# Kernel tuning notes

Hardware: AMD Instinct MI355X
Metric: run time of the kernel (lower is better)

## Reference

```python
import jax, jax.numpy as jnp
import numpy as np

D_MODEL = 768
NHEAD = 12
D_K = D_MODEL // NHEAD
D_FF = 3072
EPS = 1e-6


def layer_norm(x, a, b):
    # torch LayerNorm here: mean/std over last dim, std is UNBIASED (n-1), eps added to std
    n = x.shape[-1]
    m = jnp.mean(x, axis=-1, keepdims=True)
    var = jnp.sum((x - m) ** 2, axis=-1, keepdims=True) / (n - 1)
    return a * (x - m) / (jnp.sqrt(var) + EPS) + b


def setup_inputs() -> dict:
    key = jax.random.key(0)
    ks = jax.random.split(key, 12)
    B, S = 2, 2048
    s = 1.0 / np.sqrt(D_MODEL)
    inp = {
        'x': jax.random.normal(ks[0], (B, S, D_MODEL), jnp.float32),
        'mask': jnp.ones((B, 1, S), jnp.int32),
        'Wq': jax.random.normal(ks[1], (D_MODEL, D_MODEL), jnp.float32) * s,
        'bq': jnp.zeros((D_MODEL,), jnp.float32),
        'Wk': jax.random.normal(ks[2], (D_MODEL, D_MODEL), jnp.float32) * s,
        'bk': jnp.zeros((D_MODEL,), jnp.float32),
        'Wv': jax.random.normal(ks[3], (D_MODEL, D_MODEL), jnp.float32) * s,
        'bv': jnp.zeros((D_MODEL,), jnp.float32),
        'Wo': jax.random.normal(ks[4], (D_MODEL, D_MODEL), jnp.float32) * s,
        'bo': jnp.zeros((D_MODEL,), jnp.float32),
        'ln1_a': jnp.ones((D_MODEL,), jnp.float32),
        'ln1_b': jnp.zeros((D_MODEL,), jnp.float32),
        'W1': jax.random.normal(ks[5], (D_MODEL, D_FF), jnp.float32) * s,
        'b1': jnp.zeros((D_FF,), jnp.float32),
        'W2': jax.random.normal(ks[6], (D_FF, D_MODEL), jnp.float32) * (1.0 / np.sqrt(D_FF)),
        'b2': jnp.zeros((D_MODEL,), jnp.float32),
        'ln2_a': jnp.ones((D_MODEL,), jnp.float32),
        'ln2_b': jnp.zeros((D_MODEL,), jnp.float32),
    }
    return inp


def reference(x, mask, Wq, bq, Wk, bk, Wv, bv, Wo, bo, ln1_a, ln1_b, W1, b1, W2, b2, ln2_a, ln2_b):
    B, S, _ = x.shape
    # --- sublayer 1: pre-norm self-attention + residual (dropout = eval/no-op) ---
    h = layer_norm(x, ln1_a, ln1_b)
    q = (h @ Wq + bq).reshape(B, S, NHEAD, D_K).transpose(0, 2, 1, 3)  # [B,H,S,Dk]
    k = (h @ Wk + bk).reshape(B, S, NHEAD, D_K).transpose(0, 2, 1, 3)
    v = (h @ Wv + bv).reshape(B, S, NHEAD, D_K).transpose(0, 2, 1, 3)
    scores = jnp.einsum('bhqd,bhkd->bhqk', q, k) / np.sqrt(D_K)  # [B,H,S,S]
    scores = jnp.where(mask[:, None] == 0, jnp.float32(-1e9), scores)
    attn = jax.nn.softmax(scores, axis=-1)
    ctx = jnp.einsum('bhqk,bhkd->bhqd', attn, v)  # [B,H,S,Dk]
    ctx = ctx.transpose(0, 2, 1, 3).reshape(B, S, D_MODEL)
    x = x + (ctx @ Wo + bo)
    # --- sublayer 2: pre-norm FFN + residual ---
    h2 = layer_norm(x, ln2_a, ln2_b)
    ff = jax.nn.relu(h2 @ W1 + b1) @ W2 + b2
    return x + ff
```

## Files before the change

kernel.cpp:

```cpp
#include <hip/hip_runtime.h>
#include <hip/hip_bf16.h>
#include <stdint.h>

#define DM 768
#define DFF 3072
#define NH 12
#define DK 64
#define SS 2048
#define NTOK 4096
#define KCH 2

typedef __hip_bfloat16 bf16;
typedef short bf16x8 __attribute__((ext_vector_type(8)));
typedef float f32x4 __attribute__((ext_vector_type(4)));

#define MFMA16(a, b, c) __builtin_amdgcn_mfma_f32_16x16x32_bf16((a), (b), (c), 0, 0, 0)

#define QSCALE 0.18033688011112042f

#if __has_builtin(__builtin_amdgcn_exp2f)
#define EXP2F(x) __builtin_amdgcn_exp2f(x)
#else
#define EXP2F(x) exp2f(x)
#endif

static __device__ __forceinline__ bf16 f2b(float f) { return __float2bfloat16(f); }
static __device__ __forceinline__ unsigned short f2b_bits(float f) {
    bf16 h = __float2bfloat16(f);
    return *reinterpret_cast<unsigned short*>(&h);
}
static __device__ __forceinline__ float b2f(bf16 h) { return __bfloat162float(h); }

static __device__ __forceinline__ void g2l16(const void* g, void* l) {
    __builtin_amdgcn_global_load_lds(
        (const __attribute__((address_space(1))) unsigned int*)g,
        (__attribute__((address_space(3))) unsigned int*)(uintptr_t)l,
        16, 0, 0);
}

__global__ __launch_bounds__(256) void transpose_all(const float* Wq, const float* Wk,
                                                     const float* Wv, const float* Wo,
                                                     const float* W1, const float* W2,
                                                     bf16* WqT, bf16* WkT, bf16* WvT,
                                                     bf16* WoT, bf16* W1T, bf16* W2T) {
    __shared__ float tile[32][33];
    int id = blockIdx.x;
    const float* W; bf16* WT; int K, N, n0, k0;
    if (id < 2304) {
        int z = id / 576, r = id % 576;
        W  = (z == 0) ? Wq : (z == 1) ? Wk : (z == 2) ? Wv : Wo;
        WT = (z == 0) ? WqT : (z == 1) ? WkT : (z == 2) ? WvT : WoT;
        K = 768; N = 768; n0 = (r % 24) * 32; k0 = (r / 24) * 32;
    } else if (id < 4608) {
        int r = id - 2304; W = W1; WT = W1T;
        K = 768; N = 3072; n0 = (r % 96) * 32; k0 = (r / 96) * 32;
    } else {
        int r = id - 4608; W = W2; WT = W2T;
        K = 3072; N = 768; n0 = (r % 24) * 32; k0 = (r / 24) * 32;
    }
    int tx = threadIdx.x & 31, ty = threadIdx.x >> 5;
#pragma unroll
    for (int r = ty; r < 32; r += 8)
        tile[r][tx] = W[(size_t)(k0 + r) * N + n0 + tx];
    __syncthreads();
#pragma unroll
    for (int r = ty; r < 32; r += 8)
        WT[(size_t)(n0 + r) * K + k0 + tx] = f2b(tile[tx][r]);
}

__global__ __launch_bounds__(256) void ln_fwd(const float* __restrict__ x,
                                              const float* __restrict__ g,
                                              const float* __restrict__ be,
                                              bf16* __restrict__ out) {
    int wid = threadIdx.x >> 6, lane = threadIdx.x & 63;
    int row = blockIdx.x * 4 + wid;
    const float* xr = x + (size_t)row * DM;
    float v[12];
    float s = 0.f;
#pragma unroll
    for (int i = 0; i < 12; ++i) { v[i] = xr[lane + i * 64]; s += v[i]; }
#pragma unroll
    for (int off = 32; off >= 1; off >>= 1) s += __shfl_xor(s, off);
    float mean = s * (1.f / 768.f);
    float s2 = 0.f;
#pragma unroll
    for (int i = 0; i < 12; ++i) { float d = v[i] - mean; s2 += d * d; }
#pragma unroll
    for (int off = 32; off >= 1; off >>= 1) s2 += __shfl_xor(s2, off);
    float rstd = 1.f / (sqrtf(s2 * (1.f / 767.f)) + 1e-6f);
    bf16* orow = out + (size_t)row * DM;
#pragma unroll
    for (int i = 0; i < 12; ++i) {
        int c = lane + i * 64;
        orow[c] = f2b(g[c] * (v[i] - mean) * rstd + be[c]);
    }
}

__device__ __forceinline__ void gemm_core(const bf16* __restrict__ A,
                                          const bf16* __restrict__ BT,
                                          int K, int bm, int bn,
                                          bf16* As, bf16* Bs,
                                          f32x4 acc[4][4]) {
    int tid = threadIdx.x;
    int lane = tid & 63, quad = lane >> 4, lid = lane & 15;
    int wid = tid >> 6;
    int wm = (wid >> 1) * 64, wn = (wid & 1) * 64;
    int s0 = tid, s1 = tid + 256;
    int r0 = s0 >> 2, c0 = (s0 & 3) ^ ((r0 >> 1) & 3);
    int r1 = s1 >> 2, c1 = (s1 & 3) ^ ((r1 >> 1) & 3);
    const bf16* A0 = A + (size_t)(bm + r0) * K + c0 * 8;
    const bf16* A1 = A + (size_t)(bm + r1) * K + c1 * 8;
    const bf16* B0 = BT + (size_t)(bn + r0) * K + c0 * 8;
    const bf16* B1 = BT + (size_t)(bn + r1) * K + c1 * 8;
    int rdc = quad ^ ((lid >> 1) & 3);
    g2l16(A0, As + s0 * 8);
    g2l16(B0, Bs + s0 * 8);
    g2l16(A1, As + s1 * 8);
    g2l16(B1, Bs + s1 * 8);
    for (int k0 = 0; k0 < K; k0 += 32) {
        __syncthreads();
        int cur = (k0 >> 5) & 1;
        if (k0 + 32 < K) {
            int nb = (cur ^ 1) * 4096;
            g2l16(A0 + k0 + 32, As + nb + s0 * 8);
            g2l16(B0 + k0 + 32, Bs + nb + s0 * 8);
            g2l16(A1 + k0 + 32, As + nb + s1 * 8);
            g2l16(B1 + k0 + 32, Bs + nb + s1 * 8);
        }
        const bf16* Ac = As + cur * 4096;
        const bf16* Bc = Bs + cur * 4096;
        bf16x8 af[4], bfr[4];
#pragma unroll
        for (int i = 0; i < 4; ++i) af[i]  = *(const bf16x8*)&Ac[(wm + i * 16 + lid) * 32 + rdc * 8];
#pragma unroll
        for (int j = 0; j < 4; ++j) bfr[j] = *(const bf16x8*)&Bc[(wn + j * 16 + lid) * 32 + rdc * 8];
#pragma unroll
        for (int i = 0; i < 4; ++i)
#pragma unroll
            for (int j = 0; j < 4; ++j)
                acc[i][j] = MFMA16(af[i], bfr[j], acc[i][j]);
    }
}

__global__ __launch_bounds__(256) void gemm_qkv(const bf16* __restrict__ A,
                                                const bf16* __restrict__ WqT,
                                                const bf16* __restrict__ WkT,
                                                const bf16* __restrict__ WvT,
                                                const float* __restrict__ bq,
                                                const float* __restrict__ bk,
                                                const float* __restrict__ bv,
                                                bf16* __restrict__ qb,
                                                bf16* __restrict__ kb,
                                                bf16* __restrict__ vtb) {
    __shared__ bf16 As[2 * 128 * 32];
    __shared__ bf16 Bs[2 * 128 * 32];
    int which = blockIdx.x / 6;
    int bn = (blockIdx.x % 6) * 128;
    int bm = blockIdx.y * 128;
    const bf16* BT = (which == 0) ? WqT : (which == 1) ? WkT : WvT;
    const float* bias = (which == 0) ? bq : (which == 1) ? bk : bv;
    f32x4 acc[4][4] = {};
    gemm_core(A, BT, DM, bm, bn, As, Bs, acc);

    int tid = threadIdx.x, wid = tid >> 6, lane = tid & 63, quad = lane >> 4, lid = lane & 15;
    int wm = (wid >> 1) * 64, wn = (wid & 1) * 64;
    float sc = (which == 0) ? QSCALE : 1.f;
#pragma unroll
    for (int j = 0; j < 4; ++j) {
        int col = bn + wn + j * 16 + lid;
        float bb = bias[col];
        int hh = col >> 6, d = col & 63;
#pragma unroll
        for (int i = 0; i < 4; ++i) {
            int rowbase = bm + wm + i * 16 + quad * 4;
            int b = rowbase >> 11;
            int s0 = rowbase & 2047;
            if (which == 2) {
                ushort4 pk;
                pk.x = f2b_bits(acc[i][j][0] + bb);
                pk.y = f2b_bits(acc[i][j][1] + bb);
                pk.z = f2b_bits(acc[i][j][2] + bb);
                pk.w = f2b_bits(acc[i][j][3] + bb);
                *(ushort4*)&vtb[(((size_t)b * NH + hh) * DK + d) * SS + s0] = pk;
            } else {
                bf16* dst = which ? kb : qb;
#pragma unroll
                for (int r = 0; r < 4; ++r)
                    dst[(((size_t)b * NH + hh) * SS + (s0 + r)) * DK + d] = f2b((acc[i][j][r] + bb) * sc);
            }
        }
    }
}

template <int EPI>
__global__ __launch_bounds__(256) void gemm_ep(const bf16* __restrict__ A,
                                               const bf16* __restrict__ BT,
                                               const float* __restrict__ bias,
                                               const float* __restrict__ res,
                                               void* __restrict__ outp,
                                               int N, int K) {
    __shared__ bf16 As[2 * 128 * 32];
    __shared__ bf16 Bs[2 * 128 * 32];
    int bm = blockIdx.y * 128, bn = blockIdx.x * 128;
    f32x4 acc[4][4] = {};
    gemm_core(A, BT, K, bm, bn, As, Bs, acc);

    int tid = threadIdx.x, wid = tid >> 6, lane = tid & 63, quad = lane >> 4, lid = lane & 15;
    int wm = (wid >> 1) * 64, wn = (wid & 1) * 64;
#pragma unroll
    for (int j = 0; j < 4; ++j) {
        int col = bn + wn + j * 16 + lid;
        float bb = bias[col];
#pragma unroll
        for (int i = 0; i < 4; ++i) {
#pragma unroll
            for (int r = 0; r < 4; ++r) {
                int row = bm + wm + i * 16 + quad * 4 + r;
                float v = acc[i][j][r] + bb;
                if (EPI == 2) {
                    ((float*)outp)[(size_t)row * N + col] = res[(size_t)row * N + col] + v;
                } else {
                    ((bf16*)outp)[(size_t)row * N + col] = f2b(fmaxf(v, 0.f));
                }
            }
        }
    }
}

template <int EPI>
__global__ __launch_bounds__(256) void gemm_ep64(const bf16* __restrict__ A,
                                                 const bf16* __restrict__ BT,
                                                 const float* __restrict__ bias,
                                                 const float* __restrict__ res,
                                                 void* __restrict__ outp,
                                                 int N, int K) {
    __shared__ bf16 As[2 * 64 * 32];
    __shared__ bf16 Bs[2 * 128 * 32];
    int bm = blockIdx.y * 64, bn = blockIdx.x * 128;
    int tid = threadIdx.x, wid = tid >> 6, lane = tid & 63, quad = lane >> 4, lid = lane & 15;
    int wm = (wid >> 1) * 32, wn = (wid & 1) * 64;
    f32x4 acc[2][4] = {};
    int ra = tid >> 2, ca = (tid & 3) ^ ((ra >> 1) & 3);
    int s0 = tid, s1 = tid + 256;
    int rb0 = s0 >> 2, cb0 = (s0 & 3) ^ ((rb0 >> 1) & 3);
    int rb1 = s1 >> 2, cb1 = (s1 & 3) ^ ((rb1 >> 1) & 3);
    const bf16* Ap = A + (size_t)(bm + ra) * K + ca * 8;
    const bf16* B0 = BT + (size_t)(bn + rb0) * K + cb0 * 8;
    const bf16* B1 = BT + (size_t)(bn + rb1) * K + cb1 * 8;
    int rdc = quad ^ ((lid >> 1) & 3);
    g2l16(Ap, As + tid * 8);
    g2l16(B0, Bs + s0 * 8);
    g2l16(B1, Bs + s1 * 8);
    for (int k0 = 0; k0 < K; k0 += 32) {
        __syncthreads();
        int cur = (k0 >> 5) & 1;
        if (k0 + 32 < K) {
            g2l16(Ap + k0 + 32, As + (cur ^ 1) * 2048 + tid * 8);
            g2l16(B0 + k0 + 32, Bs + (cur ^ 1) * 4096 + s0 * 8);
            g2l16(B1 + k0 + 32, Bs + (cur ^ 1) * 4096 + s1 * 8);
        }
        const bf16* Ac = As + cur * 2048;
        const bf16* Bc = Bs + cur * 4096;
        bf16x8 af[2], bfr[4];
#pragma unroll
        for (int i = 0; i < 2; ++i) af[i]  = *(const bf16x8*)&Ac[(wm + i * 16 + lid) * 32 + rdc * 8];
#pragma unroll
        for (int j = 0; j < 4; ++j) bfr[j] = *(const bf16x8*)&Bc[(wn + j * 16 + lid) * 32 + rdc * 8];
#pragma unroll
        for (int i = 0; i < 2; ++i)
#pragma unroll
            for (int j = 0; j < 4; ++j)
                acc[i][j] = MFMA16(af[i], bfr[j], acc[i][j]);
    }
#pragma unroll
    for (int j = 0; j < 4; ++j) {
        int col = bn + wn + j * 16 + lid;
        float bb = bias[col];
#pragma unroll
        for (int i = 0; i < 2; ++i) {
#pragma unroll
            for (int r = 0; r < 4; ++r) {
                int row = bm + wm + i * 16 + quad * 4 + r;
                float v = acc[i][j][r] + bb;
                if (EPI == 2) {
                    ((float*)outp)[(size_t)row * N + col] = res[(size_t)row * N + col] + v;
                } else {
                    ((bf16*)outp)[(size_t)row * N + col] = f2b(fmaxf(v, 0.f));
                }
            }
        }
    }
}

__global__ __launch_bounds__(256) void attn_part(const bf16* __restrict__ qb,
                                                 const bf16* __restrict__ kb,
                                                 const bf16* __restrict__ vtb,
                                                 const int* __restrict__ mask,
                                                 bf16* __restrict__ part,
                                                 float* __restrict__ lws) {
    __shared__ bf16 Ks[2 * 64 * 64];
    __shared__ bf16 VTs[2 * 64 * 64];
    __shared__ bf16 Ps[64 * 72];
    int bh = blockIdx.y;
    int b = bh / NH;
    int q0 = blockIdx.x * 64;
    int kc = blockIdx.z;
    const bf16* Kp = kb  + (size_t)bh * SS * DK;
    const bf16* VT = vtb + (size_t)bh * DK * SS;
    int tid = threadIdx.x, wid = tid >> 6, lane = tid & 63, quad = lane >> 4, lid = lane & 15;

    int s0 = tid, s1 = tid + 256;
    int r0 = s0 >> 3, c0 = (s0 & 7) ^ (r0 & 7);
    int r1 = s1 >> 3, c1 = (s1 & 7) ^ (r1 & 7);

    const bf16* Qrow = qb + ((size_t)bh * SS + q0 + wid * 16 + lid) * DK;
    bf16x8 qf0 = *(const bf16x8*)&Qrow[quad * 8];
    bf16x8 qf1 = *(const bf16x8*)&Qrow[32 + quad * 8];

    bf16x8 ones;
#pragma unroll
    for (int i = 0; i < 8; ++i) ones[i] = (short)0x3F80;

    int rdc  = quad ^ (lid & 7);
    int rdc2 = rdc ^ 4;
    const int* mrow = mask + b * SS;

    f32x4 accv[4] = {};
    f32x4 accl = {};

    int tbeg = kc * (SS / 64 / KCH), tend = (kc + 1) * (SS / 64 / KCH);

    {
        int k0 = tbeg * 64;
        g2l16(Kp + (size_t)(k0 + r0) * DK + c0 * 8, Ks + s0 * 8);
        g2l16(Kp + (size_t)(k0 + r1) * DK + c1 * 8, Ks + s1 * 8);
        g2l16(VT + (size_t)r0 * SS + k0 + c0 * 8, VTs + s0 * 8);
        g2l16(VT + (size_t)r1 * SS + k0 + c1 * 8, VTs + s1 * 8);
    }

    int cur = 0;
    for (int t = tbeg; t < tend; ++t) {
        int k0 = t * 64;
        __syncthreads();
        if (t + 1 < tend) {
            int k0n = (t + 1) * 64;
            int nb = (cur ^ 1) * 4096;
            g2l16(Kp + (size_t)(k0n + r0) * DK + c0 * 8, Ks + nb + s0 * 8);
            g2l16(Kp + (size_t)(k0n + r1) * DK + c1 * 8, Ks + nb + s1 * 8);
            g2l16(VT + (size_t)r0 * SS + k0n + c0 * 8, VTs + nb + s0 * 8);
            g2l16(VT + (size_t)r1 * SS + k0n + c1 * 8, VTs + nb + s1 * 8);
        }
        const bf16* Kc  = Ks  + cur * 4096;
        const bf16* VTc = VTs + cur * 4096;

#pragma unroll
        for (int ns = 0; ns < 4; ++ns) {
            bf16x8 kf0 = *(const bf16x8*)&Kc[(ns * 16 + lid) * 64 + rdc * 8];
            bf16x8 kf1 = *(const bf16x8*)&Kc[(ns * 16 + lid) * 64 + rdc2 * 8];
            f32x4 st = {};
            st = MFMA16(kf0, qf0, st);
            st = MFMA16(kf1, qf1, st);
            int4 mk = *(const int4*)&mrow[k0 + ns * 16 + quad * 4];
            float p0 = mk.x ? EXP2F(st[0]) : 0.f;
            float p1 = mk.y ? EXP2F(st[1]) : 0.f;
            float p2 = mk.z ? EXP2F(st[2]) : 0.f;
            float p3 = mk.w ? EXP2F(st[3]) : 0.f;
            __hip_bfloat162 h01 = __float22bfloat162_rn(make_float2(p0, p1));
            __hip_bfloat162 h23 = __float22bfloat162_rn(make_float2(p2, p3));
            uint2 pw;
            pw.x = *(unsigned int*)&h01;
            pw.y = *(unsigned int*)&h23;
            *(uint2*)&Ps[(wid * 16 + lid) * 72 + ns * 16 + quad * 4] = pw;
        }

        bf16x8 pa0 = *(const bf16x8*)&Ps[(wid * 16 + lid) * 72 + quad * 8];
        bf16x8 pa1 = *(const bf16x8*)&Ps[(wid * 16 + lid) * 72 + 32 + quad * 8];

        accl = MFMA16(pa0, ones, accl);
        accl = MFMA16(pa1, ones, accl);

#pragma unroll
        for (int ds = 0; ds < 4; ++ds) {
            bf16x8 vf0 = *(const bf16x8*)&VTc[(ds * 16 + lid) * 64 + rdc * 8];
            bf16x8 vf1 = *(const bf16x8*)&VTc[(ds * 16 + lid) * 64 + rdc2 * 8];
            accv[ds] = MFMA16(pa0, vf0, accv[ds]);
            accv[ds] = MFMA16(pa1, vf1, accv[ds]);
        }
        cur ^= 1;
    }

    if (lid == 0) {
#pragma unroll
        for (int r = 0; r < 4; ++r)
            lws[((size_t)kc * (2 * NH) + bh) * SS + q0 + wid * 16 + quad * 4 + r] = accl[r];
    }

    bf16* pb = part + ((size_t)kc * (2 * NH) + bh) * DK * SS;
    int qbase = q0 + wid * 16 + quad * 4;
#pragma unroll
    for (int ds = 0; ds < 4; ++ds) {
        int d = ds * 16 + lid;
        ushort4 pk;
        pk.x = f2b_bits(accv[ds][0]);
        pk.y = f2b_bits(accv[ds][1]);
        pk.z = f2b_bits(accv[ds][2]);
        pk.w = f2b_bits(accv[ds][3]);
        *(ushort4*)&pb[(size_t)d * SS + qbase] = pk;
    }
}

__global__ __launch_bounds__(256) void attn_combine(const bf16* __restrict__ part,
                                                    const float* __restrict__ lws,
                                                    bf16* __restrict__ ctx) {
    __shared__ float tile[64][66];
    __shared__ float linv[64];
    int bh = blockIdx.y;
    int b = bh / NH, h = bh % NH;
    int q0 = blockIdx.x * 64;
    int tid = threadIdx.x;

    if (tid < 64) {
        float l = 0.f;
#pragma unroll
        for (int kc = 0; kc < KCH; ++kc)
            l += lws[((size_t)kc * (2 * NH) + bh) * SS + q0 + tid];
        linv[tid] = 1.f / l;
    }

    int d = tid >> 2, qs = (tid & 3) * 16;
    const bf16* p0 = part + (((size_t)0 * (2 * NH) + bh) * DK + d) * SS + q0 + qs;
    const bf16* p1 = part + (((size_t)1 * (2 * NH) + bh) * DK + d) * SS + q0 + qs;
    bf16x8 a0 = *(const bf16x8*)p0;
    bf16x8 a1 = *(const bf16x8*)(p0 + 8);
    bf16x8 b0 = *(const bf16x8*)p1;
    bf16x8 b1 = *(const bf16x8*)(p1 + 8);
#pragma unroll
    for (int i = 0; i < 8; ++i) {
        tile[d][qs + i]     = b2f(((const bf16*)&a0)[i]) + b2f(((const bf16*)&b0)[i]);
        tile[d][qs + 8 + i] = b2f(((const bf16*)&a1)[i]) + b2f(((const bf16*)&b1)[i]);
    }
    __syncthreads();

    int q = tid >> 2, ds2 = (tid & 3) * 16;
    float rl = linv[q];
    unsigned int wv[8];
#pragma unroll
    for (int i = 0; i < 8; ++i) {
        __hip_bfloat162 hh = __float22bfloat162_rn(
            make_float2(tile[ds2 + 2 * i][q] * rl, tile[ds2 + 2 * i + 1][q] * rl));
        wv[i] = *(unsigned int*)&hh;
    }
    bf16* crow = ctx + (size_t)(b * SS + q0 + q) * DM + h * DK + ds2;
    uint4 u0 = {wv[0], wv[1], wv[2], wv[3]};
    uint4 u1 = {wv[4], wv[5], wv[6], wv[7]};
    *(uint4*)&crow[0] = u0;
    *(uint4*)&crow[8] = u1;
}

extern "C" void kernel_launch(void* const* d_in, const int* in_sizes, int n_in,
                              void* d_out, int out_size, void* d_ws, size_t ws_size,
                              hipStream_t stream) {
    const float* x    = (const float*)d_in[0];
    const int*   mask = (const int*)d_in[1];
    const float* Wq   = (const float*)d_in[2];
    const float* bq   = (const float*)d_in[3];
    const float* Wk   = (const float*)d_in[4];
    const float* bk   = (const float*)d_in[5];
    const float* Wv   = (const float*)d_in[6];
    const float* bv   = (const float*)d_in[7];
    const float* Wo   = (const float*)d_in[8];
    const float* bo   = (const float*)d_in[9];
    const float* ln1a = (const float*)d_in[10];
    const float* ln1b = (const float*)d_in[11];
    const float* W1   = (const float*)d_in[12];
    const float* b1   = (const float*)d_in[13];
    const float* W2   = (const float*)d_in[14];
    const float* b2   = (const float*)d_in[15];
    const float* ln2a = (const float*)d_in[16];
    const float* ln2b = (const float*)d_in[17];
    float* out = (float*)d_out;

    char* w = (char*)d_ws;
    bf16* h   = (bf16*)w; w += (size_t)NTOK * DM * 2;
    bf16* qb  = (bf16*)w; w += (size_t)NTOK * DM * 2;
    bf16* kb  = (bf16*)w; w += (size_t)NTOK * DM * 2;
    bf16* vtb = (bf16*)w; w += (size_t)NTOK * DM * 2;
    bf16* ctx = (bf16*)w; w += (size_t)NTOK * DM * 2;
    bf16* h2  = (bf16*)w; w += (size_t)NTOK * DM * 2;
    bf16* ffa = (bf16*)w; w += (size_t)NTOK * DFF * 2;
    float* x1 = (float*)w; w += (size_t)NTOK * DM * 4;
    bf16* WqT = (bf16*)w; w += (size_t)DM * DM * 2;
    bf16* WkT = (bf16*)w; w += (size_t)DM * DM * 2;
    bf16* WvT = (bf16*)w; w += (size_t)DM * DM * 2;
    bf16* WoT = (bf16*)w; w += (size_t)DM * DM * 2;
    bf16* W1T = (bf16*)w; w += (size_t)DM * DFF * 2;
    bf16* W2T = (bf16*)w; w += (size_t)DM * DFF * 2;

    bf16*  part = ffa;
    float* lws  = x1;

    transpose_all<<<6912, 256, 0, stream>>>(Wq, Wk, Wv, Wo, W1, W2,
                                            WqT, WkT, WvT, WoT, W1T, W2T);

    ln_fwd<<<NTOK / 4, 256, 0, stream>>>(x, ln1a, ln1b, h);
    gemm_qkv<<<dim3(18, 32), 256, 0, stream>>>(h, WqT, WkT, WvT, bq, bk, bv, qb, kb, vtb);
    attn_part<<<dim3(SS / 64, 2 * NH, KCH), 256, 0, stream>>>(qb, kb, vtb, mask, part, lws);
    attn_combine<<<dim3(SS / 64, 2 * NH), 256, 0, stream>>>(part, lws, ctx);
    gemm_ep64<2><<<dim3(6, 64), 256, 0, stream>>>(ctx, WoT, bo, x, (void*)x1, DM, DM);
    ln_fwd<<<NTOK / 4, 256, 0, stream>>>(x1, ln2a, ln2b, h2);
    gemm_ep<3><<<dim3(24, 32), 256, 0, stream>>>(h2, W1T, b1, nullptr, (void*)ffa, DFF, DM);
    gemm_ep64<2><<<dim3(6, 64), 256, 0, stream>>>(ffa, W2T, b2, x1, (void*)out, DM, DFF);
}
```

Before: 298.8 us.

## Process 128 query rows per attention block to reuse K/V tiles

Each attention_part block now covers 128 queries instead of 64, with every wave computing two 16-row query sub-tiles against each K/V tile staged in shared memory. This halves the global-to-LDS traffic of K and V per query and reuses the K/V fragment reads across two MFMA streams. The grid shrinks to 16x24x2 = 768 blocks, which lowers parallelism on a large-CU GPU, and register pressure rises from the doubled accumulators.

```diff
diff --git a/kernel.cpp b/kernel.cpp
--- a/kernel.cpp
+++ b/kernel.cpp
@@ -300,10 +300,10 @@
                                                  float* __restrict__ lws) {
     __shared__ bf16 Ks[2 * 64 * 64];
     __shared__ bf16 VTs[2 * 64 * 64];
-    __shared__ bf16 Ps[64 * 72];
+    __shared__ bf16 Ps[128 * 72];
     int bh = blockIdx.y;
     int b = bh / NH;
-    int q0 = blockIdx.x * 64;
+    int q0 = blockIdx.x * 128;
     int kc = blockIdx.z;
     const bf16* Kp = kb  + (size_t)bh * SS * DK;
     const bf16* VT = vtb + (size_t)bh * DK * SS;
@@ -313,9 +313,13 @@
     int r0 = s0 >> 3, c0 = (s0 & 7) ^ (r0 & 7);
     int r1 = s1 >> 3, c1 = (s1 & 7) ^ (r1 & 7);
 
-    const bf16* Qrow = qb + ((size_t)bh * SS + q0 + wid * 16 + lid) * DK;
-    bf16x8 qf0 = *(const bf16x8*)&Qrow[quad * 8];
-    bf16x8 qf1 = *(const bf16x8*)&Qrow[32 + quad * 8];
+    bf16x8 qf0[2], qf1[2];
+#pragma unroll
+    for (int u = 0; u < 2; ++u) {
+        const bf16* Qrow = qb + ((size_t)bh * SS + q0 + wid * 32 + u * 16 + lid) * DK;
+        qf0[u] = *(const bf16x8*)&Qrow[quad * 8];
+        qf1[u] = *(const bf16x8*)&Qrow[32 + quad * 8];
+    }
 
     bf16x8 ones;
 #pragma unroll
@@ -325,8 +329,8 @@
     int rdc2 = rdc ^ 4;
     const int* mrow = mask + b * SS;
 
-    f32x4 accv[4] = {};
-    f32x4 accl = {};
+    f32x4 accv[2][4] = {};
+    f32x4 accl[2] = {};
 
     int tbeg = kc * (SS / 64 / KCH), tend = (kc + 1) * (SS / 64 / KCH);
 
@@ -357,55 +361,66 @@
         for (int ns = 0; ns < 4; ++ns) {
             bf16x8 kf0 = *(const bf16x8*)&Kc[(ns * 16 + lid) * 64 + rdc * 8];
             bf16x8 kf1 = *(const bf16x8*)&Kc[(ns * 16 + lid) * 64 + rdc2 * 8];
-            f32x4 st = {};
-            st = MFMA16(kf0, qf0, st);
-            st = MFMA16(kf1, qf1, st);
             int4 mk = *(const int4*)&mrow[k0 + ns * 16 + quad * 4];
-            float p0 = mk.x ? EXP2F(st[0]) : 0.f;
-            float p1 = mk.y ? EXP2F(st[1]) : 0.f;
-            float p2 = mk.z ? EXP2F(st[2]) : 0.f;
-            float p3 = mk.w ? EXP2F(st[3]) : 0.f;
-            __hip_bfloat162 h01 = __float22bfloat162_rn(make_float2(p0, p1));
-            __hip_bfloat162 h23 = __float22bfloat162_rn(make_float2(p2, p3));
-            uint2 pw;
-            pw.x = *(unsigned int*)&h01;
-            pw.y = *(unsigned int*)&h23;
-            *(uint2*)&Ps[(wid * 16 + lid) * 72 + ns * 16 + quad * 4] = pw;
-        }
-
-        bf16x8 pa0 = *(const bf16x8*)&Ps[(wid * 16 + lid) * 72 + quad * 8];
-        bf16x8 pa1 = *(const bf16x8*)&Ps[(wid * 16 + lid) * 72 + 32 + quad * 8];
-
-        accl = MFMA16(pa0, ones, accl);
-        accl = MFMA16(pa1, ones, accl);
+#pragma unroll
+            for (int u = 0; u < 2; ++u) {
+                f32x4 st = {};
+                st = MFMA16(kf0, qf0[u], st);
+                st = MFMA16(kf1, qf1[u], st);
+                float p0 = mk.x ? EXP2F(st[0]) : 0.f;
+                float p1 = mk.y ? EXP2F(st[1]) : 0.f;
+                float p2 = mk.z ? EXP2F(st[2]) : 0.f;
+                float p3 = mk.w ? EXP2F(st[3]) : 0.f;
+                __hip_bfloat162 h01 = __float22bfloat162_rn(make_float2(p0, p1));
+                __hip_bfloat162 h23 = __float22bfloat162_rn(make_float2(p2, p3));
+                uint2 pw;
+                pw.x = *(unsigned int*)&h01;
+                pw.y = *(unsigned int*)&h23;
+                *(uint2*)&Ps[(wid * 32 + u * 16 + lid) * 72 + ns * 16 + quad * 4] = pw;
+            }
+        }
+
+        bf16x8 pa0[2], pa1[2];
+#pragma unroll
+        for (int u = 0; u < 2; ++u) {
+            pa0[u] = *(const bf16x8*)&Ps[(wid * 32 + u * 16 + lid) * 72 + quad * 8];
+            pa1[u] = *(const bf16x8*)&Ps[(wid * 32 + u * 16 + lid) * 72 + 32 + quad * 8];
+            accl[u] = MFMA16(pa0[u], ones, accl[u]);
+            accl[u] = MFMA16(pa1[u], ones, accl[u]);
+        }
 
 #pragma unroll
         for (int ds = 0; ds < 4; ++ds) {
             bf16x8 vf0 = *(const bf16x8*)&VTc[(ds * 16 + lid) * 64 + rdc * 8];
             bf16x8 vf1 = *(const bf16x8*)&VTc[(ds * 16 + lid) * 64 + rdc2 * 8];
-            accv[ds] = MFMA16(pa0, vf0, accv[ds]);
-            accv[ds] = MFMA16(pa1, vf1, accv[ds]);
+#pragma unroll
+            for (int u = 0; u < 2; ++u) {
+                accv[u][ds] = MFMA16(pa0[u], vf0, accv[u][ds]);
+                accv[u][ds] = MFMA16(pa1[u], vf1, accv[u][ds]);
+            }
         }
         cur ^= 1;
     }
 
-    if (lid == 0) {
-#pragma unroll
-        for (int r = 0; r < 4; ++r)
-            lws[((size_t)kc * (2 * NH) + bh) * SS + q0 + wid * 16 + quad * 4 + r] = accl[r];
-    }
-
     bf16* pb = part + ((size_t)kc * (2 * NH) + bh) * DK * SS;
-    int qbase = q0 + wid * 16 + quad * 4;
-#pragma unroll
-    for (int ds = 0; ds < 4; ++ds) {
-        int d = ds * 16 + lid;
-        ushort4 pk;
-        pk.x = f2b_bits(accv[ds][0]);
-        pk.y = f2b_bits(accv[ds][1]);
-        pk.z = f2b_bits(accv[ds][2]);
-        pk.w = f2b_bits(accv[ds][3]);
-        *(ushort4*)&pb[(size_t)d * SS + qbase] = pk;
+#pragma unroll
+    for (int u = 0; u < 2; ++u) {
+        if (lid == 0) {
+#pragma unroll
+            for (int r = 0; r < 4; ++r)
+                lws[((size_t)kc * (2 * NH) + bh) * SS + q0 + wid * 32 + u * 16 + quad * 4 + r] = accl[u][r];
+        }
+        int qbase = q0 + wid * 32 + u * 16 + quad * 4;
+#pragma unroll
+        for (int ds = 0; ds < 4; ++ds) {
+            int d = ds * 16 + lid;
+            ushort4 pk;
+            pk.x = f2b_bits(accv[u][ds][0]);
+            pk.y = f2b_bits(accv[u][ds][1]);
+            pk.z = f2b_bits(accv[u][ds][2]);
+            pk.w = f2b_bits(accv[u][ds][3]);
+            *(ushort4*)&pb[(size_t)d * SS + qbase] = pk;
+        }
     }
 }
 
@@ -504,7 +519,7 @@
 
     ln_fwd<<<NTOK / 4, 256, 0, stream>>>(x, ln1a, ln1b, h);
     gemm_qkv<<<dim3(18, 32), 256, 0, stream>>>(h, WqT, WkT, WvT, bq, bk, bv, qb, kb, vtb);
-    attn_part<<<dim3(SS / 64, 2 * NH, KCH), 256, 0, stream>>>(qb, kb, vtb, mask, part, lws);
+    attn_part<<<dim3(SS / 128, 2 * NH, KCH), 256, 0, stream>>>(qb, kb, vtb, mask, part, lws);
     attn_combine<<<dim3(SS / 64, 2 * NH), 256, 0, stream>>>(part, lws, ctx);
     gemm_ep64<2><<<dim3(6, 64), 256, 0, stream>>>(ctx, WoT, bo, x, (void*)x1, DM, DM);
     ln_fwd<<<NTOK / 4, 256, 0, stream>>>(x1, ln2a, ln2b, h2);
```

Result: faster. 291.0 us (-2.6%).
